# Kernel tuning notes

Hardware: AMD Instinct MI355X
Metric: run time of the kernel (lower is better)

Reference implementation:

```python
import jax, jax.numpy as jnp
import numpy as np
import math

B, C, H, W, D = 4, 64, 16, 16, 16
TEMB = 256
GROUPS = 16
EPS = 1e-5


def group_norm(x, gamma, beta, groups=GROUPS, eps=EPS):
    # x: [B, C, H, W, D]
    b, c, h, w, d = x.shape
    xg = x.reshape(b, groups, c // groups, h, w, d)
    mu = jnp.mean(xg, axis=(2, 3, 4, 5), keepdims=True)
    var = jnp.var(xg, axis=(2, 3, 4, 5), keepdims=True)
    xn = ((xg - mu) / jnp.sqrt(var + eps)).reshape(b, c, h, w, d)
    return xn * gamma[None, :, None, None, None] + beta[None, :, None, None, None]


def swish(x):
    return x * jax.nn.sigmoid(x)


def conv3d(x, w, b=None):
    y = jax.lax.conv_general_dilated(
        x, w, window_strides=(1, 1, 1), padding='SAME',
        dimension_numbers=('NCDHW', 'OIDHW', 'NCDHW'))
    if b is not None:
        y = y + b[None, :, None, None, None]
    return y


def setup_inputs() -> dict:
    key = jax.random.key(0)
    ks = jax.random.split(key, 16)
    s = lambda fan: 1.0 / math.sqrt(fan)
    inp = {
        'x': jax.random.normal(ks[0], (B, C, H, W, D), jnp.float32),
        'time_emb': jax.random.normal(ks[1], (B, TEMB), jnp.float32),
        # block1: GroupNorm + Conv3d(C->C, 3)
        'gn1_g': jnp.ones((C,), jnp.float32),
        'gn1_b': jnp.zeros((C,), jnp.float32),
        'conv1_w': jax.random.normal(ks[2], (C, C, 3, 3, 3), jnp.float32) * s(C * 27),
        'conv1_b': jnp.zeros((C,), jnp.float32),
        # time-embedding MLP: Linear(TEMB -> C)
        'mlp_w': jax.random.normal(ks[3], (C, TEMB), jnp.float32) * s(TEMB),
        'mlp_b': jnp.zeros((C,), jnp.float32),
        # block2: GroupNorm + Conv3d(C->C, 3)
        'gn2_g': jnp.ones((C,), jnp.float32),
        'gn2_b': jnp.zeros((C,), jnp.float32),
        'conv2_w': jax.random.normal(ks[4], (C, C, 3, 3, 3), jnp.float32) * s(C * 27),
        'conv2_b': jnp.zeros((C,), jnp.float32),
        # attention: GroupNorm, qkv 1x1 conv (no bias), out 1x1 conv
        'agn_g': jnp.ones((C,), jnp.float32),
        'agn_b': jnp.zeros((C,), jnp.float32),
        'qkv_w': jax.random.normal(ks[5], (3 * C, C), jnp.float32) * s(C),
        'out_w': jax.random.normal(ks[6], (C, C), jnp.float32) * s(C),
        'out_b': jnp.zeros((C,), jnp.float32),
    }
    return inp


def reference(x, time_emb, gn1_g, gn1_b, conv1_w, conv1_b, mlp_w, mlp_b,
              gn2_g, gn2_b, conv2_w, conv2_b, agn_g, agn_b, qkv_w, out_w, out_b):
    # --- ResnetBlock ---
    h = conv3d(swish(group_norm(x, gn1_g, gn1_b)), conv1_w, conv1_b)
    t = swish(time_emb) @ mlp_w.T + mlp_b                    # [B, C]
    h = h + t[:, :, None, None, None]
    h = conv3d(swish(group_norm(h, gn2_g, gn2_b)), conv2_w, conv2_b)
    x = h + x                                                # res_conv is Identity (dim == dim_out)
    # --- SelfAttention (n_head = 1) ---
    b, c, hh, ww, dd = x.shape
    n = hh * ww * dd
    norm = group_norm(x, agn_g, agn_b)
    qkv = jnp.einsum('oc,bchwd->bohwd', qkv_w, norm).reshape(b, 3 * c, n)
    q, k, v = jnp.split(qkv, 3, axis=1)                      # [B, C, N] each
    attn = jnp.einsum('bcn,bcm->bnm', q, k) / math.sqrt(c)   # [B, N, N]
    attn = jax.nn.softmax(attn, axis=-1)
    o = jnp.einsum('bnm,bcm->bcn', attn, v).reshape(b, c, hh, ww, dd)
    o = jnp.einsum('oc,bchwd->bohwd', out_w, o) + out_b[None, :, None, None, None]
    return o + x
```

## Files before the change

### kernel.cpp

```cpp
#include <hip/hip_runtime.h>
#include <math.h>

#define B 4
#define C 64
#define G 16
#define CPG 4
#define N 4096
#define TEMB 256

using f16x8 = __attribute__((ext_vector_type(8))) _Float16;
using f16x4 = __attribute__((ext_vector_type(4))) _Float16;
using f32x4 = __attribute__((ext_vector_type(4))) float;
using f32x16 = __attribute__((ext_vector_type(16))) float;
using h2 = __attribute__((ext_vector_type(2))) __fp16;

#define QSCALE 0.18033688f
#define SHIFT2 4.328085f

__device__ __forceinline__ int swzi(int row, int ci) {
  return (((ci >> 3) ^ (row & 7)) << 3) | (ci & 7);
}

__device__ __forceinline__ void gn_fin(const float2* pstats, const float* gamma,
                                       const float* beta, int b, int c,
                                       float& sc, float& sh) {
  int g = c >> 2;
  const float2* ps = pstats + ((size_t)(b * 16 + g)) * 4;
  float2 p0 = ps[0], p1 = ps[1], p2 = ps[2], p3 = ps[3];
  const float inv = 1.f / 16384.f;
  float mean = (p0.x + p1.x + p2.x + p3.x) * inv;
  float msq = (p0.y + p1.y + p2.y + p3.y) * inv;
  float var = msq - mean * mean;
  float rstd = rsqrtf(var + 1e-5f);
  sc = gamma[c] * rstd;
  sh = beta[c] - mean * sc;
}

__global__ void __launch_bounds__(256) k_gnpart(const float* __restrict__ x,
                                                float2* __restrict__ pstats) {
  int bx = blockIdx.x;
  const float4* xp = (const float4*)(x + (size_t)bx * 4096);
  float s = 0.f, s2 = 0.f;
#pragma unroll
  for (int kk = 0; kk < 4; kk++) {
    float4 v = xp[threadIdx.x + kk * 256];
    s += v.x + v.y + v.z + v.w;
    s2 += v.x * v.x + v.y * v.y + v.z * v.z + v.w * v.w;
  }
#pragma unroll
  for (int off = 32; off > 0; off >>= 1) {
    s += __shfl_down(s, off);
    s2 += __shfl_down(s2, off);
  }
  __shared__ float ls[4], ls2[4];
  int lane = threadIdx.x & 63, wid = threadIdx.x >> 6;
  if (lane == 0) { ls[wid] = s; ls2[wid] = s2; }
  __syncthreads();
  if (threadIdx.x == 0) {
    float2 r;
    r.x = ls[0] + ls[1] + ls[2] + ls[3];
    r.y = ls2[0] + ls2[1] + ls2[2] + ls2[3];
    pstats[bx] = r;
  }
}

__global__ void __launch_bounds__(256) k_prep(const float* __restrict__ w1,
                                              const float* __restrict__ w2,
                                              const float* __restrict__ temb,
                                              const float* __restrict__ mlp_w,
                                              const float* __restrict__ mlp_b,
                                              _Float16* __restrict__ wf1,
                                              _Float16* __restrict__ wf2,
                                              float* __restrict__ tb) {
  int bx = blockIdx.x, tid = threadIdx.x;
  if (bx < 54) {
    const float* w = (bx < 27) ? w1 : w2;
    _Float16* wf = (bx < 27) ? wf1 : wf2;
    int tap = (bx < 27) ? bx : bx - 27;
    int co = tid >> 2, ci0 = (tid & 3) * 16;
    union { _Float16 hh[16]; f16x8 v[2]; } pk;
#pragma unroll
    for (int r = 0; r < 16; r++)
      pk.hh[r] = (_Float16)w[((size_t)(co * 64 + ci0 + r)) * 27 + tap];
    f16x8* dst = (f16x8*)(wf + ((size_t)tap * 64 + co) * 64 + ci0);
    dst[0] = pk.v[0]; dst[1] = pk.v[1];
  } else {
    int b = bx - 54;
    __shared__ float sw[TEMB];
    __shared__ float part[4][64];
    {
      float v = temb[b * TEMB + tid];
      sw[tid] = v / (1.f + __expf(-v));
    }
    __syncthreads();
    int co = tid & 63, seg = tid >> 6;
    float acc = 0.f;
#pragma unroll 16
    for (int k = 0; k < 64; k++) acc += sw[seg * 64 + k] * mlp_w[co * TEMB + seg * 64 + k];
    part[seg][co] = acc;
    __syncthreads();
    if (tid < 64) tb[b * C + tid] = part[0][tid] + part[1][tid] + part[2][tid] + part[3][tid] + mlp_b[tid];
  }
}

__global__ void __launch_bounds__(256) k_actT(const float* __restrict__ in,
                                              const float2* __restrict__ pstats,
                                              const float* __restrict__ gamma,
                                              const float* __restrict__ beta,
                                              _Float16* __restrict__ outT) {
  int b = blockIdx.x >> 6, nt = blockIdx.x & 63;
  int n0 = nt * 64;
  __shared__ float xl[64][68];
  int tid = threadIdx.x;
  {
    int c = tid >> 2, seg = tid & 3;
    float sc, sh;
    gn_fin(pstats, gamma, beta, b, c, sc, sh);
    const float4* src = (const float4*)(in + ((size_t)(b * C + c)) * N + n0 + seg * 16);
#pragma unroll
    for (int j = 0; j < 4; j++) {
      float4 v = src[j];
      float t0 = v.x * sc + sh, t1 = v.y * sc + sh, t2 = v.z * sc + sh, t3 = v.w * sc + sh;
      xl[c][seg * 16 + j * 4 + 0] = t0 / (1.f + __expf(-t0));
      xl[c][seg * 16 + j * 4 + 1] = t1 / (1.f + __expf(-t1));
      xl[c][seg * 16 + j * 4 + 2] = t2 / (1.f + __expf(-t2));
      xl[c][seg * 16 + j * 4 + 3] = t3 / (1.f + __expf(-t3));
    }
  }
  __syncthreads();
  {
    int n = tid >> 2, cq = (tid & 3) * 16;
    union { _Float16 hh[16]; f16x8 v[2]; } pk;
#pragma unroll
    for (int r = 0; r < 16; r++) pk.hh[r] = (_Float16)xl[cq + r][n];
    f16x8* dst = (f16x8*)(outT + ((size_t)b * N + n0 + n) * 64 + cq);
    dst[0] = pk.v[0]; dst[1] = pk.v[1];
  }
}

__global__ void __launch_bounds__(256) k_conv3(const _Float16* __restrict__ actT,
                                               const _Float16* __restrict__ wf,
                                               const float* __restrict__ bias,
                                               const float* __restrict__ addvec,
                                               const float* __restrict__ residual,
                                               float* __restrict__ out) {
  int bx = blockIdx.x;
  int b = bx >> 6, h = (bx >> 2) & 15, nog = bx & 3;
  int tid = threadIdx.x;
  int wv = tid >> 6, lane = tid & 63, hi = lane >> 5, l31 = lane & 31;
  int cw = wv >> 1, nw = wv & 1;
  __shared__ _Float16 a3[3][96][64];
  __shared__ _Float16 wl[2][64][64];
  int w0 = nog * 4 - 1;
  for (int idx = tid; idx < 2304; idx += 256) {
    int r = idx / 768, rem = idx % 768;
    int ns = rem >> 3, ci8 = rem & 7;
    int wp = w0 + (ns >> 4), dp = ns & 15;
    int hin = h + r - 1;
    f16x8 v = {};
    if ((unsigned)hin < 16u && (unsigned)wp < 16u)
      v = *(const f16x8*)(actT + (((size_t)(b * 16 + hin)) * 256 + wp * 16 + dp) * 64 + ci8 * 8);
    *(f16x8*)&a3[r][ns][swzi(ns, ci8 * 8)] = v;
  }
#pragma unroll
  for (int q = 0; q < 2; q++) {
    int chunk = tid + q * 256;
    int co = chunk >> 3, ci8 = chunk & 7;
    f16x8 v = *(const f16x8*)(wf + (size_t)co * 64 + ci8 * 8);
    *(f16x8*)&wl[0][co][swzi(co, ci8 * 8)] = v;
  }
  f32x16 acc = {};
  __syncthreads();
  int cur = 0;
  int co_r = cw * 32 + l31;
  int n_loc = nw * 32 + l31;
  int wrow = n_loc >> 4;
  int d = n_loc & 15;
  for (int t = 0; t < 27; t++) {
    f16x8 pw0 = {}, pw1 = {};
    if (t < 26) {
      pw0 = *(const f16x8*)(wf + ((size_t)(t + 1) * 64 + (tid >> 3)) * 64 + (tid & 7) * 8);
      pw1 = *(const f16x8*)(wf + ((size_t)(t + 1) * 64 + ((tid + 256) >> 3)) * 64 + (tid & 7) * 8);
    }
    int kw = (t / 3) % 3, kd = t % 3, kh = t / 9;
    int wpl = wrow + kw;
    int dp = d + kd - 1;
    bool ok = (unsigned)dp < 16u;
    int ns = wpl * 16 + dp;
#pragma unroll
    for (int c4 = 0; c4 < 4; c4++) {
      int ci = c4 * 16 + hi * 8;
      f16x8 af = *(const f16x8*)&wl[cur][co_r][swzi(co_r, ci)];
      f16x8 bf = {};
      if (ok) bf = *(const f16x8*)&a3[kh][ns][swzi(ns, ci)];
      acc = __builtin_amdgcn_mfma_f32_32x32x16_f16(af, bf, acc, 0, 0, 0);
    }
    if (t < 26) {
      *(f16x8*)&wl[cur ^ 1][tid >> 3][swzi(tid >> 3, (tid & 7) * 8)] = pw0;
      *(f16x8*)&wl[cur ^ 1][(tid + 256) >> 3][swzi((tid + 256) >> 3, (tid & 7) * 8)] = pw1;
      __syncthreads();
      cur ^= 1;
    }
  }
  int nq = nog * 64 + n_loc;
#pragma unroll
  for (int r = 0; r < 16; r++) {
    int co = cw * 32 + (r & 3) + 8 * (r >> 2) + 4 * hi;
    size_t off = (((size_t)(b * 64 + co)) * 16 + h) * 256 + nq;
    float vv = acc[r] + bias[co] + (addvec ? addvec[b * 64 + co] : 0.f);
    if (residual) vv += residual[off];
    out[off] = vv;
  }
}

__global__ void __launch_bounds__(256) k_qkv(const float* __restrict__ x2,
                                             const float2* __restrict__ pstats,
                                             const float* __restrict__ gamma,
                                             const float* __restrict__ beta,
                                             const float* __restrict__ w,
                                             _Float16* __restrict__ qh, _Float16* __restrict__ kh,
                                             _Float16* __restrict__ vh) {
  int b = blockIdx.x >> 6, nt = blockIdx.x & 63;
  int n0 = nt * 64;
  __shared__ __align__(16) float xl[64][64];
  __shared__ float wl[192 * 64];
  int tid = threadIdx.x;
  for (int i = tid; i < 192 * 64; i += 256) wl[i] = w[i];
  {
    int c = tid >> 2, seg = tid & 3;
    float sc, sh;
    gn_fin(pstats, gamma, beta, b, c, sc, sh);
    const float4* src = (const float4*)(x2 + ((size_t)(b * C + c)) * N + n0);
    float4* dst = (float4*)&xl[c][seg * 16];
#pragma unroll
    for (int j = 0; j < 4; j++) {
      float4 v = src[seg * 4 + j];
      v.x = v.x * sc + sh; v.y = v.y * sc + sh; v.z = v.z * sc + sh; v.w = v.w * sc + sh;
      dst[j] = v;
    }
  }
  __syncthreads();
  int nq = tid & 15, og = tid >> 4;
  float4 acc[12];
#pragma unroll
  for (int j = 0; j < 12; j++) acc[j] = make_float4(0.f, 0.f, 0.f, 0.f);
  for (int c = 0; c < 64; c++) {
    float4 xv = *(const float4*)&xl[c][nq * 4];
#pragma unroll
    for (int j = 0; j < 12; j++) {
      float wv = wl[(og * 12 + j) * 64 + c];
      acc[j].x += wv * xv.x; acc[j].y += wv * xv.y; acc[j].z += wv * xv.z; acc[j].w += wv * xv.w;
    }
  }
#pragma unroll
  for (int j = 0; j < 12; j++) {
    int o3 = og * 12 + j;
    if (o3 >= 128) {
      f16x4 pv;
      pv[0] = (_Float16)acc[j].x; pv[1] = (_Float16)acc[j].y;
      pv[2] = (_Float16)acc[j].z; pv[3] = (_Float16)acc[j].w;
      int c = o3 - 128;
      int t = (n0 >> 4) + (nq >> 2);
      *(f16x4*)(vh + ((size_t)(b * 256 + t) * 64 + c) * 16 + (nq & 3) * 4) = pv;
    }
  }
  __syncthreads();
#pragma unroll
  for (int j = 0; j < 12; j++) {
    int o3 = og * 12 + j;
    if (o3 < 64) {
      float4 v = acc[j];
      v.x *= QSCALE; v.y *= QSCALE; v.z *= QSCALE; v.w *= QSCALE;
      *(float4*)&xl[o3][nq * 4] = v;
    }
  }
  __syncthreads();
  {
    int n_ = tid >> 2, cs = (tid & 3) * 16;
    union { _Float16 hh[16]; uint4 u[2]; } pk;
#pragma unroll
    for (int r = 0; r < 16; r++) pk.hh[r] = (_Float16)xl[cs + r][n_];
    uint4* dst = (uint4*)(qh + ((size_t)b * N + n0 + n_) * 64 + cs);
    dst[0] = pk.u[0]; dst[1] = pk.u[1];
  }
  __syncthreads();
#pragma unroll
  for (int j = 0; j < 12; j++) {
    int o3 = og * 12 + j;
    if (o3 >= 64 && o3 < 128) *(float4*)&xl[o3 - 64][nq * 4] = acc[j];
  }
  __syncthreads();
  {
    int n_ = tid >> 2, cs = (tid & 3) * 16;
    union { _Float16 hh[16]; uint4 u[2]; } pk;
#pragma unroll
    for (int r = 0; r < 16; r++) pk.hh[r] = (_Float16)xl[cs + r][n_];
    uint4* dst = (uint4*)(kh + ((size_t)b * N + n0 + n_) * 64 + cs);
    dst[0] = pk.u[0]; dst[1] = pk.u[1];
  }
}

__global__ void __launch_bounds__(256) k_attn(const _Float16* __restrict__ q,
                                              const _Float16* __restrict__ k,
                                              const _Float16* __restrict__ v,
                                              _Float16* __restrict__ po,
                                              float* __restrict__ pl) {
  int bx = blockIdx.x;
  int s = bx >> 8, b = (bx >> 6) & 3, nt = bx & 63;
  int n0 = nt * 64;
  int tid = threadIdx.x;
  int wv = tid >> 6, lane = tid & 63, lg = lane >> 4, ll = lane & 15;
  __shared__ float ol[64][72];
  __shared__ float lsum[4][64];
  const _Float16* qp = q + (size_t)b * N * 64;
  f16x8 qf[4][2];
#pragma unroll
  for (int qb = 0; qb < 4; qb++)
#pragma unroll
    for (int ch = 0; ch < 2; ch++)
      qf[qb][ch] = *(const f16x8*)(qp + (size_t)(n0 + qb * 16 + ll) * 64 + ch * 32 + lg * 8);
  f32x4 oacc[4][4] = {};
  f32x4 lfrag[4] = {};
  const f16x4 ones = {(_Float16)1.f, (_Float16)1.f, (_Float16)1.f, (_Float16)1.f};
  const _Float16* kptr = k + (size_t)b * N * 64 + (size_t)(s * 1024 + wv * 16 + ll) * 64 + lg * 8;
  const _Float16* vptr = v + ((size_t)(b * 256 + s * 64 + wv) * 64 + ll) * 16 + lg * 4;
  f16x8 kf0 = *(const f16x8*)(kptr);
  f16x8 kf1 = *(const f16x8*)(kptr + 32);
  f16x4 vf[4];
#pragma unroll
  for (int cb = 0; cb < 4; cb++) vf[cb] = *(const f16x4*)(vptr + cb * 256);
  for (int it = 0; it < 16; it++) {
    const _Float16* kptrn = kptr + 4096;
    const _Float16* vptrn = vptr + 4096;
    f32x4 sv[4];
    __builtin_amdgcn_s_setprio(1);
#pragma unroll
    for (int qb = 0; qb < 4; qb++) {
      f32x4 z = {-SHIFT2, -SHIFT2, -SHIFT2, -SHIFT2};
      z = __builtin_amdgcn_mfma_f32_16x16x32_f16(kf0, qf[qb][0], z, 0, 0, 0);
      sv[qb] = __builtin_amdgcn_mfma_f32_16x16x32_f16(kf1, qf[qb][1], z, 0, 0, 0);
    }
    __builtin_amdgcn_s_setprio(0);
    f16x8 nk0 = *(const f16x8*)(kptrn);
    f16x8 nk1 = *(const f16x8*)(kptrn + 32);
    f16x4 nv[4];
#pragma unroll
    for (int cb = 0; cb < 4; cb++) nv[cb] = *(const f16x4*)(vptrn + cb * 256);
    f16x4 pk[4];
#pragma unroll
    for (int qb = 0; qb < 4; qb++) {
      float e0 = __builtin_amdgcn_exp2f(sv[qb][0]);
      float e1 = __builtin_amdgcn_exp2f(sv[qb][1]);
      float e2 = __builtin_amdgcn_exp2f(sv[qb][2]);
      float e3 = __builtin_amdgcn_exp2f(sv[qb][3]);
      union { h2 h[2]; f16x4 v4; } u;
      u.h[0] = __builtin_amdgcn_cvt_pkrtz(e0, e1);
      u.h[1] = __builtin_amdgcn_cvt_pkrtz(e2, e3);
      pk[qb] = u.v4;
    }
    __builtin_amdgcn_s_setprio(1);
#pragma unroll
    for (int qb = 0; qb < 4; qb++) {
#pragma unroll
      for (int cb = 0; cb < 4; cb++)
        oacc[qb][cb] = __builtin_amdgcn_mfma_f32_16x16x16f16(vf[cb], pk[qb], oacc[qb][cb], 0, 0, 0);
      lfrag[qb] = __builtin_amdgcn_mfma_f32_16x16x16f16(ones, pk[qb], lfrag[qb], 0, 0, 0);
    }
    __builtin_amdgcn_s_setprio(0);
    kf0 = nk0; kf1 = nk1;
#pragma unroll
    for (int cb = 0; cb < 4; cb++) vf[cb] = nv[cb];
    kptr = kptrn; vptr = vptrn;
  }
  if (lane < 16) {
#pragma unroll
    for (int qb = 0; qb < 4; qb++) lsum[wv][qb * 16 + lane] = lfrag[qb][0];
  }
  for (int w = 0; w < 4; w++) {
    __syncthreads();
    if (wv == w) {
#pragma unroll
      for (int qb = 0; qb < 4; qb++)
#pragma unroll
        for (int cb = 0; cb < 4; cb++) {
          float* a = &ol[qb * 16 + ll][cb * 16 + 4 * lg];
          if (w == 0) {
            *(f32x4*)a = oacc[qb][cb];
          } else {
            f32x4 t = *(f32x4*)a;
            t += oacc[qb][cb];
            *(f32x4*)a = t;
          }
        }
    }
  }
  __syncthreads();
  {
    int n = tid >> 2, cq = (tid & 3) * 16;
    float lt = lsum[0][n] + lsum[1][n] + lsum[2][n] + lsum[3][n];
    float inv = 1.f / lt;
    union { _Float16 hh[16]; uint4 u[2]; } pk2;
#pragma unroll
    for (int j = 0; j < 16; j++) pk2.hh[j] = (_Float16)(ol[n][cq + j] * inv);
    uint4* dst = (uint4*)(po + ((size_t)(s * 4 + b) * N + n0 + n) * 64 + cq);
    dst[0] = pk2.u[0]; dst[1] = pk2.u[1];
    if (tid < 64)
      pl[(size_t)(s * 4 + b) * N + n0 + tid] =
          lsum[0][tid] + lsum[1][tid] + lsum[2][tid] + lsum[3][tid];
  }
}

__global__ void __launch_bounds__(256) k_outproj(const _Float16* __restrict__ po,
                                                 const float* __restrict__ pl,
                                                 const float* __restrict__ w,
                                                 const float* __restrict__ bias,
                                                 const float* __restrict__ x2,
                                                 float* __restrict__ out) {
  int b = blockIdx.x >> 6, nt = blockIdx.x & 63;
  int n0 = nt * 64;
  __shared__ __align__(16) float wl2[64][68];
  __shared__ __align__(16) float ol[64][68];
  __shared__ float wsc[4][64];
  int tid = threadIdx.x;
  if (tid < 64) {
    float l0 = pl[((size_t)(0 * 4 + b)) * N + n0 + tid];
    float l1 = pl[((size_t)(1 * 4 + b)) * N + n0 + tid];
    float l2 = pl[((size_t)(2 * 4 + b)) * N + n0 + tid];
    float l3 = pl[((size_t)(3 * 4 + b)) * N + n0 + tid];
    float inv = 1.f / (l0 + l1 + l2 + l3);
    wsc[0][tid] = l0 * inv; wsc[1][tid] = l1 * inv;
    wsc[2][tid] = l2 * inv; wsc[3][tid] = l3 * inv;
  }
  for (int i = tid; i < 4096; i += 256) wl2[i >> 6][i & 63] = w[i];
  __syncthreads();
  for (int i = tid; i < 4096; i += 256) {
    int n = i >> 6, c = i & 63;
    float acc = 0.f;
#pragma unroll
    for (int s = 0; s < 4; s++)
      acc += (float)po[((size_t)(s * 4 + b) * N + n0 + n) * 64 + c] * wsc[s][n];
    ol[n][c] = acc;
  }
  __syncthreads();
  int co = tid & 63, ng = tid >> 6;
  float acc16[16];
#pragma unroll
  for (int i = 0; i < 16; i++) acc16[i] = 0.f;
  for (int c4 = 0; c4 < 16; c4++) {
    float4 wv = *(const float4*)&wl2[co][c4 * 4];
#pragma unroll
    for (int i = 0; i < 16; i++) {
      float4 ov = *(const float4*)&ol[ng * 16 + i][c4 * 4];
      acc16[i] += wv.x * ov.x + wv.y * ov.y + wv.z * ov.z + wv.w * ov.w;
    }
  }
  float bv = bias[co];
  __syncthreads();
#pragma unroll
  for (int i = 0; i < 16; i++) ol[ng * 16 + i][co] = acc16[i] + bv;
  __syncthreads();
  for (int kk = 0; kk < 16; kk++) {
    int i = tid + kk * 256;
    int c2 = i >> 6, nl = i & 63;
    size_t idx = ((size_t)(b * C + c2)) * N + n0 + nl;
    out[idx] = ol[nl][c2] + x2[idx];
  }
}

extern "C" void kernel_launch(void* const* d_in, const int* in_sizes, int n_in,
                              void* d_out, int out_size, void* d_ws, size_t ws_size,
                              hipStream_t stream) {
  (void)in_sizes; (void)n_in; (void)out_size; (void)ws_size;
  const float* x       = (const float*)d_in[0];
  const float* temb    = (const float*)d_in[1];
  const float* gn1_g   = (const float*)d_in[2];
  const float* gn1_b   = (const float*)d_in[3];
  const float* conv1_w = (const float*)d_in[4];
  const float* conv1_b = (const float*)d_in[5];
  const float* mlp_w   = (const float*)d_in[6];
  const float* mlp_b   = (const float*)d_in[7];
  const float* gn2_g   = (const float*)d_in[8];
  const float* gn2_b   = (const float*)d_in[9];
  const float* conv2_w = (const float*)d_in[10];
  const float* conv2_b = (const float*)d_in[11];
  const float* agn_g   = (const float*)d_in[12];
  const float* agn_b   = (const float*)d_in[13];
  const float* qkv_w   = (const float*)d_in[14];
  const float* out_w   = (const float*)d_in[15];
  const float* out_b   = (const float*)d_in[16];
  float* out = (float*)d_out;
  float* ws = (float*)d_ws;
  const size_t F = 1048576;
  float* h        = ws;
  _Float16* qh    = (_Float16*)(ws + F);
  _Float16* khb   = qh + F;
  _Float16* vhb   = khb + F;
  float2* pst1 = (float2*)(vhb + F);
  float2* pst2 = pst1 + 256;
  float2* pst3 = pst2 + 256;
  float* tb    = (float*)(pst3 + 256);
  _Float16* wf1 = (_Float16*)(tb + 256);
  _Float16* wf2 = wf1 + 27 * 64 * 64;
  _Float16* actT = wf2 + 27 * 64 * 64;
  _Float16* po   = actT;
  float* pl      = (float*)(po + 4 * F);

  k_prep<<<58, 256, 0, stream>>>(conv1_w, conv2_w, temb, mlp_w, mlp_b, wf1, wf2, tb);
  k_gnpart<<<256, 256, 0, stream>>>(x, pst1);
  k_actT<<<256, 256, 0, stream>>>(x, pst1, gn1_g, gn1_b, actT);
  k_conv3<<<256, 256, 0, stream>>>(actT, wf1, conv1_b, tb, nullptr, h);
  k_gnpart<<<256, 256, 0, stream>>>(h, pst2);
  k_actT<<<256, 256, 0, stream>>>(h, pst2, gn2_g, gn2_b, actT);
  k_conv3<<<256, 256, 0, stream>>>(actT, wf2, conv2_b, nullptr, x, h);
  k_gnpart<<<256, 256, 0, stream>>>(h, pst3);
  k_qkv<<<256, 256, 0, stream>>>(h, pst3, agn_g, agn_b, qkv_w, qh, khb, vhb);
  k_attn<<<1024, 256, 0, stream>>>(qh, khb, vhb, po, pl);
  k_outproj<<<256, 256, 0, stream>>>(po, pl, out_w, out_b, h, out);
}
```

Before: 116.3 us.

## Fuse group-norm stats into conv epilogue and split attention keys eightfold

New measurement: 128.2 us. 1.1x slower.

```diff
diff --git a/kernel.cpp b/kernel.cpp
--- a/kernel.cpp
+++ b/kernel.cpp
@@ -36,6 +36,18 @@
   sh = beta[c] - mean * sc;
 }
 
+__device__ __forceinline__ void gn_fin2(const float2* red, const float* gamma,
+                                        const float* beta, int b, int c,
+                                        float& sc, float& sh) {
+  float2 r = red[b * 16 + (c >> 2)];
+  const float inv = 1.f / 16384.f;
+  float mean = r.x * inv;
+  float var = r.y * inv - mean * mean;
+  float rstd = rsqrtf(var + 1e-5f);
+  sc = gamma[c] * rstd;
+  sh = beta[c] - mean * sc;
+}
+
 __global__ void __launch_bounds__(256) k_gnpart(const float* __restrict__ x,
                                                 float2* __restrict__ pstats) {
   int bx = blockIdx.x;
@@ -62,6 +74,20 @@
     r.y = ls2[0] + ls2[1] + ls2[2] + ls2[3];
     pstats[bx] = r;
   }
+}
+
+__global__ void k_gnred(const float2* __restrict__ blkstats, float2* __restrict__ red) {
+  int tid = threadIdx.x;
+  int pair = tid >> 2, q = tid & 3;
+  int b = pair >> 4, g = pair & 15;
+  float sx = 0.f, sy = 0.f;
+  for (int i = 0; i < 16; i++) {
+    float2 v = blkstats[(size_t)(b * 64 + q * 16 + i) * 16 + g];
+    sx += v.x; sy += v.y;
+  }
+  sx += __shfl_xor(sx, 1); sy += __shfl_xor(sy, 1);
+  sx += __shfl_xor(sx, 2); sy += __shfl_xor(sy, 2);
+  if (q == 0) { float2 r; r.x = sx; r.y = sy; red[pair] = r; }
 }
 
 __global__ void __launch_bounds__(256) k_prep(const float* __restrict__ w1,
@@ -107,7 +133,7 @@
                                               const float2* __restrict__ pstats,
                                               const float* __restrict__ gamma,
                                               const float* __restrict__ beta,
-                                              _Float16* __restrict__ outT) {
+                                              _Float16* __restrict__ outT, int mode) {
   int b = blockIdx.x >> 6, nt = blockIdx.x & 63;
   int n0 = nt * 64;
   __shared__ float xl[64][68];
@@ -115,7 +141,8 @@
   {
     int c = tid >> 2, seg = tid & 3;
     float sc, sh;
-    gn_fin(pstats, gamma, beta, b, c, sc, sh);
+    if (mode == 0) gn_fin(pstats, gamma, beta, b, c, sc, sh);
+    else gn_fin2(pstats, gamma, beta, b, c, sc, sh);
     const float4* src = (const float4*)(in + ((size_t)(b * C + c)) * N + n0 + seg * 16);
 #pragma unroll
     for (int j = 0; j < 4; j++) {
@@ -143,7 +170,8 @@
                                                const float* __restrict__ bias,
                                                const float* __restrict__ addvec,
                                                const float* __restrict__ residual,
-                                               float* __restrict__ out) {
+                                               float* __restrict__ out,
+                                               float2* __restrict__ blkstats) {
   int bx = blockIdx.x;
   int b = bx >> 6, h = (bx >> 2) & 15, nog = bx & 3;
   int tid = threadIdx.x;
@@ -151,6 +179,8 @@
   int cw = wv >> 1, nw = wv & 1;
   __shared__ _Float16 a3[3][96][64];
   __shared__ _Float16 wl[2][64][64];
+  __shared__ float2 sg[16];
+  if (tid < 16) { sg[tid].x = 0.f; sg[tid].y = 0.f; }
   int w0 = nog * 4 - 1;
   for (int idx = tid; idx < 2304; idx += 256) {
     int r = idx / 768, rem = idx % 768;
@@ -203,6 +233,7 @@
     }
   }
   int nq = nog * 64 + n_loc;
+  float gs[4] = {0.f, 0.f, 0.f, 0.f}, gs2[4] = {0.f, 0.f, 0.f, 0.f};
 #pragma unroll
   for (int r = 0; r < 16; r++) {
     int co = cw * 32 + (r & 3) + 8 * (r >> 2) + 4 * hi;
@@ -210,11 +241,30 @@
     float vv = acc[r] + bias[co] + (addvec ? addvec[b * 64 + co] : 0.f);
     if (residual) vv += residual[off];
     out[off] = vv;
-  }
+    gs[r >> 2] += vv;
+    gs2[r >> 2] += vv * vv;
+  }
+#pragma unroll
+  for (int off2 = 1; off2 < 32; off2 <<= 1)
+#pragma unroll
+    for (int rq = 0; rq < 4; rq++) {
+      gs[rq] += __shfl_xor(gs[rq], off2);
+      gs2[rq] += __shfl_xor(gs2[rq], off2);
+    }
+  if (l31 == 0) {
+#pragma unroll
+    for (int rq = 0; rq < 4; rq++) {
+      int g = cw * 8 + 2 * rq + hi;
+      atomicAdd(&sg[g].x, gs[rq]);
+      atomicAdd(&sg[g].y, gs2[rq]);
+    }
+  }
+  __syncthreads();
+  if (tid < 16) blkstats[(size_t)bx * 16 + tid] = sg[tid];
 }
 
 __global__ void __launch_bounds__(256) k_qkv(const float* __restrict__ x2,
-                                             const float2* __restrict__ pstats,
+                                             const float2* __restrict__ red,
                                              const float* __restrict__ gamma,
                                              const float* __restrict__ beta,
                                              const float* __restrict__ w,
@@ -229,7 +279,7 @@
   {
     int c = tid >> 2, seg = tid & 3;
     float sc, sh;
-    gn_fin(pstats, gamma, beta, b, c, sc, sh);
+    gn_fin2(red, gamma, beta, b, c, sc, sh);
     const float4* src = (const float4*)(x2 + ((size_t)(b * C + c)) * N + n0);
     float4* dst = (float4*)&xl[c][seg * 16];
 #pragma unroll
@@ -322,14 +372,14 @@
   f32x4 oacc[4][4] = {};
   f32x4 lfrag[4] = {};
   const f16x4 ones = {(_Float16)1.f, (_Float16)1.f, (_Float16)1.f, (_Float16)1.f};
-  const _Float16* kptr = k + (size_t)b * N * 64 + (size_t)(s * 1024 + wv * 16 + ll) * 64 + lg * 8;
-  const _Float16* vptr = v + ((size_t)(b * 256 + s * 64 + wv) * 64 + ll) * 16 + lg * 4;
+  const _Float16* kptr = k + (size_t)b * N * 64 + (size_t)(s * 512 + wv * 16 + ll) * 64 + lg * 8;
+  const _Float16* vptr = v + ((size_t)(b * 256 + s * 32 + wv) * 64 + ll) * 16 + lg * 4;
   f16x8 kf0 = *(const f16x8*)(kptr);
   f16x8 kf1 = *(const f16x8*)(kptr + 32);
   f16x4 vf[4];
 #pragma unroll
   for (int cb = 0; cb < 4; cb++) vf[cb] = *(const f16x4*)(vptr + cb * 256);
-  for (int it = 0; it < 16; it++) {
+  for (int it = 0; it < 8; it++) {
     const _Float16* kptrn = kptr + 4096;
     const _Float16* vptrn = vptr + 4096;
     f32x4 sv[4];
@@ -420,26 +470,33 @@
   int n0 = nt * 64;
   __shared__ __align__(16) float wl2[64][68];
   __shared__ __align__(16) float ol[64][68];
-  __shared__ float wsc[4][64];
+  __shared__ float wsc[8][64];
   int tid = threadIdx.x;
   if (tid < 64) {
-    float l0 = pl[((size_t)(0 * 4 + b)) * N + n0 + tid];
-    float l1 = pl[((size_t)(1 * 4 + b)) * N + n0 + tid];
-    float l2 = pl[((size_t)(2 * 4 + b)) * N + n0 + tid];
-    float l3 = pl[((size_t)(3 * 4 + b)) * N + n0 + tid];
-    float inv = 1.f / (l0 + l1 + l2 + l3);
-    wsc[0][tid] = l0 * inv; wsc[1][tid] = l1 * inv;
-    wsc[2][tid] = l2 * inv; wsc[3][tid] = l3 * inv;
+    float l[8];
+    float lt = 0.f;
+#pragma unroll
+    for (int s = 0; s < 8; s++) {
+      l[s] = pl[((size_t)(s * 4 + b)) * N + n0 + tid];
+      lt += l[s];
+    }
+    float inv = 1.f / lt;
+#pragma unroll
+    for (int s = 0; s < 8; s++) wsc[s][tid] = l[s] * inv;
   }
   for (int i = tid; i < 4096; i += 256) wl2[i >> 6][i & 63] = w[i];
   __syncthreads();
-  for (int i = tid; i < 4096; i += 256) {
-    int n = i >> 6, c = i & 63;
-    float acc = 0.f;
-#pragma unroll
-    for (int s = 0; s < 4; s++)
-      acc += (float)po[((size_t)(s * 4 + b) * N + n0 + n) * 64 + c] * wsc[s][n];
-    ol[n][c] = acc;
+  for (int base = tid; base < 1024; base += 256) {
+    int n = base >> 4, c0 = (base & 15) * 4;
+    float a0 = 0.f, a1 = 0.f, a2 = 0.f, a3 = 0.f;
+#pragma unroll
+    for (int s = 0; s < 8; s++) {
+      f16x4 pv = *(const f16x4*)&po[((size_t)(s * 4 + b) * N + n0 + n) * 64 + c0];
+      float wsv = wsc[s][n];
+      a0 += (float)pv[0] * wsv; a1 += (float)pv[1] * wsv;
+      a2 += (float)pv[2] * wsv; a3 += (float)pv[3] * wsv;
+    }
+    ol[n][c0] = a0; ol[n][c0 + 1] = a1; ol[n][c0 + 2] = a2; ol[n][c0 + 3] = a3;
   }
   __syncthreads();
   int co = tid & 63, ng = tid >> 6;
@@ -496,24 +553,26 @@
   _Float16* khb   = qh + F;
   _Float16* vhb   = khb + F;
   float2* pst1 = (float2*)(vhb + F);
-  float2* pst2 = pst1 + 256;
-  float2* pst3 = pst2 + 256;
-  float* tb    = (float*)(pst3 + 256);
+  float* tb    = (float*)(pst1 + 256);
   _Float16* wf1 = (_Float16*)(tb + 256);
   _Float16* wf2 = wf1 + 27 * 64 * 64;
   _Float16* actT = wf2 + 27 * 64 * 64;
   _Float16* po   = actT;
-  float* pl      = (float*)(po + 4 * F);
+  float* pl      = (float*)(po + 8 * F);
+  float2* pstb1  = (float2*)(pl + 131072);
+  float2* pstb2  = pstb1 + 4096;
+  float2* red2   = pstb2 + 4096;
+  float2* red3   = red2 + 64;
 
   k_prep<<<58, 256, 0, stream>>>(conv1_w, conv2_w, temb, mlp_w, mlp_b, wf1, wf2, tb);
   k_gnpart<<<256, 256, 0, stream>>>(x, pst1);
-  k_actT<<<256, 256, 0, stream>>>(x, pst1, gn1_g, gn1_b, actT);
-  k_conv3<<<256, 256, 0, stream>>>(actT, wf1, conv1_b, tb, nullptr, h);
-  k_gnpart<<<256, 256, 0, stream>>>(h, pst2);
-  k_actT<<<256, 256, 0, stream>>>(h, pst2, gn2_g, gn2_b, actT);
-  k_conv3<<<256, 256, 0, stream>>>(actT, wf2, conv2_b, nullptr, x, h);
-  k_gnpart<<<256, 256, 0, stream>>>(h, pst3);
-  k_qkv<<<256, 256, 0, stream>>>(h, pst3, agn_g, agn_b, qkv_w, qh, khb, vhb);
-  k_attn<<<1024, 256, 0, stream>>>(qh, khb, vhb, po, pl);
+  k_actT<<<256, 256, 0, stream>>>(x, pst1, gn1_g, gn1_b, actT, 0);
+  k_conv3<<<256, 256, 0, stream>>>(actT, wf1, conv1_b, tb, nullptr, h, pstb1);
+  k_gnred<<<1, 256, 0, stream>>>(pstb1, red2);
+  k_actT<<<256, 256, 0, stream>>>(h, (const float2*)red2, gn2_g, gn2_b, actT, 1);
+  k_conv3<<<256, 256, 0, stream>>>(actT, wf2, conv2_b, nullptr, x, h, pstb2);
+  k_gnred<<<1, 256, 0, stream>>>(pstb2, red3);
+  k_qkv<<<256, 256, 0, stream>>>(h, (const float2*)red3, agn_g, agn_b, qkv_w, qh, khb, vhb);
+  k_attn<<<2048, 256, 0, stream>>>(qh, khb, vhb, po, pl);
   k_outproj<<<256, 256, 0, stream>>>(po, pl, out_w, out_b, h, out);
 }
```

## Fuse GroupNorm+swish transpose into conv loads and merge first stats pass into prep

Applied to the files above, without the earlier changes.

Measured after the change: 114.5 us. Within noise of the previous version (-1.6%).

```diff
diff --git a/kernel.cpp b/kernel.cpp
--- a/kernel.cpp
+++ b/kernel.cpp
@@ -64,15 +64,20 @@
   }
 }
 
-__global__ void __launch_bounds__(256) k_prep(const float* __restrict__ w1,
-                                              const float* __restrict__ w2,
-                                              const float* __restrict__ temb,
-                                              const float* __restrict__ mlp_w,
-                                              const float* __restrict__ mlp_b,
-                                              _Float16* __restrict__ wf1,
-                                              _Float16* __restrict__ wf2,
-                                              float* __restrict__ tb) {
+__global__ void __launch_bounds__(256) k_prepgn(const float* __restrict__ w1,
+                                                const float* __restrict__ w2,
+                                                const float* __restrict__ temb,
+                                                const float* __restrict__ mlp_w,
+                                                const float* __restrict__ mlp_b,
+                                                const float* __restrict__ x,
+                                                _Float16* __restrict__ wf1,
+                                                _Float16* __restrict__ wf2,
+                                                float* __restrict__ tb,
+                                                float2* __restrict__ pstats) {
   int bx = blockIdx.x, tid = threadIdx.x;
+  __shared__ float sw[TEMB];
+  __shared__ float part[4][64];
+  __shared__ float ls[4], ls2[4];
   if (bx < 54) {
     const float* w = (bx < 27) ? w1 : w2;
     _Float16* wf = (bx < 27) ? wf1 : wf2;
@@ -84,10 +89,8 @@
       pk.hh[r] = (_Float16)w[((size_t)(co * 64 + ci0 + r)) * 27 + tap];
     f16x8* dst = (f16x8*)(wf + ((size_t)tap * 64 + co) * 64 + ci0);
     dst[0] = pk.v[0]; dst[1] = pk.v[1];
-  } else {
+  } else if (bx < 58) {
     int b = bx - 54;
-    __shared__ float sw[TEMB];
-    __shared__ float part[4][64];
     {
       float v = temb[b * TEMB + tid];
       sw[tid] = v / (1.f + __expf(-v));
@@ -100,50 +103,42 @@
     part[seg][co] = acc;
     __syncthreads();
     if (tid < 64) tb[b * C + tid] = part[0][tid] + part[1][tid] + part[2][tid] + part[3][tid] + mlp_b[tid];
-  }
-}
-
-__global__ void __launch_bounds__(256) k_actT(const float* __restrict__ in,
-                                              const float2* __restrict__ pstats,
-                                              const float* __restrict__ gamma,
-                                              const float* __restrict__ beta,
-                                              _Float16* __restrict__ outT) {
-  int b = blockIdx.x >> 6, nt = blockIdx.x & 63;
-  int n0 = nt * 64;
-  __shared__ float xl[64][68];
-  int tid = threadIdx.x;
-  {
-    int c = tid >> 2, seg = tid & 3;
-    float sc, sh;
-    gn_fin(pstats, gamma, beta, b, c, sc, sh);
-    const float4* src = (const float4*)(in + ((size_t)(b * C + c)) * N + n0 + seg * 16);
-#pragma unroll
-    for (int j = 0; j < 4; j++) {
-      float4 v = src[j];
-      float t0 = v.x * sc + sh, t1 = v.y * sc + sh, t2 = v.z * sc + sh, t3 = v.w * sc + sh;
-      xl[c][seg * 16 + j * 4 + 0] = t0 / (1.f + __expf(-t0));
-      xl[c][seg * 16 + j * 4 + 1] = t1 / (1.f + __expf(-t1));
-      xl[c][seg * 16 + j * 4 + 2] = t2 / (1.f + __expf(-t2));
-      xl[c][seg * 16 + j * 4 + 3] = t3 / (1.f + __expf(-t3));
-    }
-  }
-  __syncthreads();
-  {
-    int n = tid >> 2, cq = (tid & 3) * 16;
-    union { _Float16 hh[16]; f16x8 v[2]; } pk;
-#pragma unroll
-    for (int r = 0; r < 16; r++) pk.hh[r] = (_Float16)xl[cq + r][n];
-    f16x8* dst = (f16x8*)(outT + ((size_t)b * N + n0 + n) * 64 + cq);
-    dst[0] = pk.v[0]; dst[1] = pk.v[1];
-  }
-}
-
-__global__ void __launch_bounds__(256) k_conv3(const _Float16* __restrict__ actT,
-                                               const _Float16* __restrict__ wf,
-                                               const float* __restrict__ bias,
-                                               const float* __restrict__ addvec,
-                                               const float* __restrict__ residual,
-                                               float* __restrict__ out) {
+  } else {
+    int bx2 = bx - 58;
+    const float4* xp = (const float4*)(x + (size_t)bx2 * 4096);
+    float s = 0.f, s2 = 0.f;
+#pragma unroll
+    for (int kk = 0; kk < 4; kk++) {
+      float4 v = xp[tid + kk * 256];
+      s += v.x + v.y + v.z + v.w;
+      s2 += v.x * v.x + v.y * v.y + v.z * v.z + v.w * v.w;
+    }
+#pragma unroll
+    for (int off = 32; off > 0; off >>= 1) {
+      s += __shfl_down(s, off);
+      s2 += __shfl_down(s2, off);
+    }
+    int lane = tid & 63, wid = tid >> 6;
+    if (lane == 0) { ls[wid] = s; ls2[wid] = s2; }
+    __syncthreads();
+    if (tid == 0) {
+      float2 r;
+      r.x = ls[0] + ls[1] + ls[2] + ls[3];
+      r.y = ls2[0] + ls2[1] + ls2[2] + ls2[3];
+      pstats[bx2] = r;
+    }
+  }
+}
+
+__global__ void __launch_bounds__(256) k_conv3f(const float* __restrict__ in,
+                                                const float2* __restrict__ pstats,
+                                                const float* __restrict__ gamma,
+                                                const float* __restrict__ beta,
+                                                const _Float16* __restrict__ wf,
+                                                const float* __restrict__ bias,
+                                                const float* __restrict__ addvec,
+                                                const float* __restrict__ residual,
+                                                float* __restrict__ out) {
   int bx = blockIdx.x;
   int b = bx >> 6, h = (bx >> 2) & 15, nog = bx & 3;
   int tid = threadIdx.x;
@@ -151,16 +146,34 @@
   int cw = wv >> 1, nw = wv & 1;
   __shared__ _Float16 a3[3][96][64];
   __shared__ _Float16 wl[2][64][64];
+  __shared__ float2 scsh[64];
+  if (tid < 64) {
+    float sc, sh;
+    gn_fin(pstats, gamma, beta, b, tid, sc, sh);
+    float2 r; r.x = sc; r.y = sh;
+    scsh[tid] = r;
+  }
+  __syncthreads();
   int w0 = nog * 4 - 1;
-  for (int idx = tid; idx < 2304; idx += 256) {
-    int r = idx / 768, rem = idx % 768;
-    int ns = rem >> 3, ci8 = rem & 7;
-    int wp = w0 + (ns >> 4), dp = ns & 15;
+  for (int i = tid; i < 2304; i += 256) {
+    int r = i / 768, rem = i % 768;
+    int ci8 = rem / 96, ns = rem % 96;
+    int wp = w0 + (ns >> 4), dd = ns & 15;
     int hin = h + r - 1;
-    f16x8 v = {};
-    if ((unsigned)hin < 16u && (unsigned)wp < 16u)
-      v = *(const f16x8*)(actT + (((size_t)(b * 16 + hin)) * 256 + wp * 16 + dp) * 64 + ci8 * 8);
-    *(f16x8*)&a3[r][ns][swzi(ns, ci8 * 8)] = v;
+    f16x8 val = {};
+    if ((unsigned)hin < 16u && (unsigned)wp < 16u) {
+      const float* src = in + (((size_t)(b * 64 + ci8 * 8) * 16 + hin) * 256) + wp * 16 + dd;
+      union { _Float16 hh[8]; f16x8 v; } pk;
+#pragma unroll
+      for (int j = 0; j < 8; j++) {
+        float v = src[(size_t)j * 4096];
+        float2 ss = scsh[ci8 * 8 + j];
+        float t = v * ss.x + ss.y;
+        pk.hh[j] = (_Float16)(t / (1.f + __expf(-t)));
+      }
+      val = pk.v;
+    }
+    *(f16x8*)&a3[r][ns][swzi(ns, ci8 * 8)] = val;
   }
 #pragma unroll
   for (int q = 0; q < 2; q++) {
@@ -433,13 +446,17 @@
   }
   for (int i = tid; i < 4096; i += 256) wl2[i >> 6][i & 63] = w[i];
   __syncthreads();
-  for (int i = tid; i < 4096; i += 256) {
-    int n = i >> 6, c = i & 63;
-    float acc = 0.f;
-#pragma unroll
-    for (int s = 0; s < 4; s++)
-      acc += (float)po[((size_t)(s * 4 + b) * N + n0 + n) * 64 + c] * wsc[s][n];
-    ol[n][c] = acc;
+  for (int base = tid; base < 1024; base += 256) {
+    int n = base >> 4, c0 = (base & 15) * 4;
+    float a0 = 0.f, a1 = 0.f, a2 = 0.f, a3 = 0.f;
+#pragma unroll
+    for (int s = 0; s < 4; s++) {
+      f16x4 pv = *(const f16x4*)&po[((size_t)(s * 4 + b) * N + n0 + n) * 64 + c0];
+      float wsv = wsc[s][n];
+      a0 += (float)pv[0] * wsv; a1 += (float)pv[1] * wsv;
+      a2 += (float)pv[2] * wsv; a3 += (float)pv[3] * wsv;
+    }
+    ol[n][c0] = a0; ol[n][c0 + 1] = a1; ol[n][c0 + 2] = a2; ol[n][c0 + 3] = a3;
   }
   __syncthreads();
   int co = tid & 63, ng = tid >> 6;
@@ -492,7 +509,8 @@
   float* ws = (float*)d_ws;
   const size_t F = 1048576;
   float* h        = ws;
-  _Float16* qh    = (_Float16*)(ws + F);
+  float* x2       = ws + F;
+  _Float16* qh    = (_Float16*)(ws + 2 * F);
   _Float16* khb   = qh + F;
   _Float16* vhb   = khb + F;
   float2* pst1 = (float2*)(vhb + F);
@@ -501,19 +519,16 @@
   float* tb    = (float*)(pst3 + 256);
   _Float16* wf1 = (_Float16*)(tb + 256);
   _Float16* wf2 = wf1 + 27 * 64 * 64;
-  _Float16* actT = wf2 + 27 * 64 * 64;
-  _Float16* po   = actT;
-  float* pl      = (float*)(po + 4 * F);
-
-  k_prep<<<58, 256, 0, stream>>>(conv1_w, conv2_w, temb, mlp_w, mlp_b, wf1, wf2, tb);
-  k_gnpart<<<256, 256, 0, stream>>>(x, pst1);
-  k_actT<<<256, 256, 0, stream>>>(x, pst1, gn1_g, gn1_b, actT);
-  k_conv3<<<256, 256, 0, stream>>>(actT, wf1, conv1_b, tb, nullptr, h);
+  _Float16* po  = wf2 + 27 * 64 * 64;
+  float* pl     = (float*)(po + 4 * F);
+
+  k_prepgn<<<314, 256, 0, stream>>>(conv1_w, conv2_w, temb, mlp_w, mlp_b, x,
+                                    wf1, wf2, tb, pst1);
+  k_conv3f<<<256, 256, 0, stream>>>(x, pst1, gn1_g, gn1_b, wf1, conv1_b, tb, nullptr, h);
   k_gnpart<<<256, 256, 0, stream>>>(h, pst2);
-  k_actT<<<256, 256, 0, stream>>>(h, pst2, gn2_g, gn2_b, actT);
-  k_conv3<<<256, 256, 0, stream>>>(actT, wf2, conv2_b, nullptr, x, h);
-  k_gnpart<<<256, 256, 0, stream>>>(h, pst3);
-  k_qkv<<<256, 256, 0, stream>>>(h, pst3, agn_g, agn_b, qkv_w, qh, khb, vhb);
+  k_conv3f<<<256, 256, 0, stream>>>(h, pst2, gn2_g, gn2_b, wf2, conv2_b, nullptr, x, x2);
+  k_gnpart<<<256, 256, 0, stream>>>(x2, pst3);
+  k_qkv<<<256, 256, 0, stream>>>(x2, pst3, agn_g, agn_b, qkv_w, qh, khb, vhb);
   k_attn<<<1024, 256, 0, stream>>>(qh, khb, vhb, po, pl);
-  k_outproj<<<256, 256, 0, stream>>>(po, pl, out_w, out_b, h, out);
-}
+  k_outproj<<<256, 256, 0, stream>>>(po, pl, out_w, out_b, x2, out);
+}
```
